# Kernel optimization log

Hardware: AMD Instinct MI355X
Metric: run time of the kernel (lower is better)

The kernel has to match this reference:

```python
import jax, jax.numpy as jnp
import numpy as np

N = 500_000   # rows in embedding matrix
D = 128       # embedding dim
B = 65_536    # number of segments (batches)
SEG = 16      # uniform segment length
T = B * SEG   # total gathered rows


def setup_inputs() -> dict:
    key = jax.random.key(0)
    k1, k2 = jax.random.split(key)
    embs = jax.random.normal(k1, (N, D), dtype=jnp.float32)
    batches = jax.random.randint(k2, (T,), 0, N, dtype=jnp.int32)
    # CSR pointer: [0, 16, 32, ..., T]; monotone, last entry == T, no empty segments
    lens = jnp.arange(B + 1, dtype=jnp.int32) * SEG
    return {"embs": embs, "batches": batches, "lens": lens}


def reference(embs, batches, lens):
    """MultiPool: gather rows then CSR-segmented sum/mean/min/max, concat on dim 1."""
    num_seg = lens.shape[0] - 1
    t = batches.shape[0]
    src = embs[batches]                                   # [T, D] gather
    # CSR pointer -> per-row segment id: seg[i] = j s.t. lens[j] <= i < lens[j+1]
    seg = jnp.searchsorted(lens, jnp.arange(t, dtype=lens.dtype), side="right") - 1
    ssum = jax.ops.segment_sum(src, seg, num_segments=num_seg)                      # [B, D]
    counts = jax.ops.segment_sum(jnp.ones((t,), src.dtype), seg, num_segments=num_seg)
    smean = ssum / jnp.maximum(counts, 1.0)[:, None]
    smin = jax.ops.segment_min(src, seg, num_segments=num_seg)
    smax = jax.ops.segment_max(src, seg, num_segments=num_seg)
    return jnp.concatenate([ssum, smean, smin, smax], axis=1)  # [B, 4*D]
```

## Files before the change

### kernel.cpp

```cpp
#include <hip/hip_runtime.h>
#include <math.h>


#ifndef INFINITY
#define INFINITY __builtin_huge_valf()
#endif

typedef float f32x4 __attribute__((ext_vector_type(4)));

constexpr int D = 128;
constexpr int LANES_PER_SEG = 32;
constexpr int SEGLEN = 16;

__global__ __launch_bounds__(256) void multipool_kernel(
    const float* __restrict__ embs,
    const int*   __restrict__ batches,
    const int*   __restrict__ lens,
    float*       __restrict__ out,
    int B)
{
    const int tid   = blockIdx.x * blockDim.x + threadIdx.x;
    const int seg   = tid >> 5;
    const int lane  = tid & 31;
    if (seg >= B) return;

    const int start = lens[seg];
    const int end   = lens[seg + 1];
    const int cnt   = end - start;

    const int col = lane * 4;

    f32x4 s  = {0.f, 0.f, 0.f, 0.f};
    f32x4 mn = { INFINITY,  INFINITY,  INFINITY,  INFINITY};
    f32x4 mx = {-INFINITY, -INFINITY, -INFINITY, -INFINITY};

    if (cnt == SEGLEN) {
        const int4* ip = reinterpret_cast<const int4*>(batches + start);
        const int4 i0 = ip[0], i1 = ip[1], i2 = ip[2], i3 = ip[3];
        const int rows[SEGLEN] = {i0.x, i0.y, i0.z, i0.w,
                                  i1.x, i1.y, i1.z, i1.w,
                                  i2.x, i2.y, i2.z, i2.w,
                                  i3.x, i3.y, i3.z, i3.w};

        f32x4 v[SEGLEN];
#pragma unroll
        for (int i = 0; i < SEGLEN; ++i) {
            const unsigned off = ((unsigned)rows[i] << 7) | (unsigned)col;
            v[i] = *reinterpret_cast<const f32x4*>(embs + off);
        }
#pragma unroll
        for (int i = 0; i < SEGLEN; ++i) {
            s += v[i];
            mn.x = fminf(mn.x, v[i].x); mn.y = fminf(mn.y, v[i].y);
            mn.z = fminf(mn.z, v[i].z); mn.w = fminf(mn.w, v[i].w);
            mx.x = fmaxf(mx.x, v[i].x); mx.y = fmaxf(mx.y, v[i].y);
            mx.z = fmaxf(mx.z, v[i].z); mx.w = fmaxf(mx.w, v[i].w);
        }
    } else {
        for (int i = start; i < end; ++i) {
            const int row = batches[i];
            const f32x4 v = *reinterpret_cast<const f32x4*>(
                embs + (size_t)row * D + col);
            s += v;
            mn.x = fminf(mn.x, v.x); mn.y = fminf(mn.y, v.y);
            mn.z = fminf(mn.z, v.z); mn.w = fminf(mn.w, v.w);
            mx.x = fmaxf(mx.x, v.x); mx.y = fmaxf(mx.y, v.y);
            mx.z = fmaxf(mx.z, v.z); mx.w = fmaxf(mx.w, v.w);
        }
    }

    const float inv = 1.0f / fmaxf((float)cnt, 1.0f);
    const f32x4 mean = s * inv;

    float* ob = out + (size_t)seg * (4 * D);
    __builtin_nontemporal_store(s,    reinterpret_cast<f32x4*>(ob + col));
    __builtin_nontemporal_store(mean, reinterpret_cast<f32x4*>(ob + D + col));
    __builtin_nontemporal_store(mn,   reinterpret_cast<f32x4*>(ob + 2 * D + col));
    __builtin_nontemporal_store(mx,   reinterpret_cast<f32x4*>(ob + 3 * D + col));
}

extern "C" void kernel_launch(void* const* d_in, const int* in_sizes, int n_in,
                              void* d_out, int out_size, void* d_ws, size_t ws_size,
                              hipStream_t stream) {
    const float* embs    = (const float*)d_in[0];
    const int*   batches = (const int*)d_in[1];
    const int*   lens    = (const int*)d_in[2];
    float*       out     = (float*)d_out;

    const int B = in_sizes[2] - 1;

    const int threads = 256;
    const long long total_threads = (long long)B * LANES_PER_SEG;
    const int blocks = (int)((total_threads + threads - 1) / threads);

    multipool_kernel<<<blocks, threads, 0, stream>>>(embs, batches, lens, out, B);
}
```

Baseline: 101.6 us.

## Map one full wavefront per segment with float2 loads and scalar row indices

Each segment is now handled by a 64-lane wavefront, with two floats per lane, instead of 32 lanes with four floats each. Segment bounds and gathered row indices are moved into scalar registers with readfirstlane, so address math becomes wave-uniform and each row load is one coalesced 512-byte access. This doubles the thread count and halves per-thread work and register use, which should raise occupancy and memory-level parallelism. The cost is more wavefronts to schedule and narrower 8-byte vector accesses per lane.

Result: faster. 95.43 us, median of 2 (-6.1%).

```diff
diff --git a/kernel.cpp b/kernel.cpp
--- a/kernel.cpp
+++ b/kernel.cpp
@@ -6,10 +6,9 @@
 #define INFINITY __builtin_huge_valf()
 #endif
 
-typedef float f32x4 __attribute__((ext_vector_type(4)));
+typedef float f32x2 __attribute__((ext_vector_type(2)));
 
 constexpr int D = 128;
-constexpr int LANES_PER_SEG = 32;
 constexpr int SEGLEN = 16;
 
 __global__ __launch_bounds__(256) void multipool_kernel(
@@ -19,20 +18,20 @@
     float*       __restrict__ out,
     int B)
 {
-    const int tid   = blockIdx.x * blockDim.x + threadIdx.x;
-    const int seg   = tid >> 5;
-    const int lane  = tid & 31;
+    const int tid  = blockIdx.x * blockDim.x + threadIdx.x;
+    const int seg  = tid >> 6;
+    const int lane = threadIdx.x & 63;
     if (seg >= B) return;
 
-    const int start = lens[seg];
-    const int end   = lens[seg + 1];
+    const int start = __builtin_amdgcn_readfirstlane(lens[seg]);
+    const int end   = __builtin_amdgcn_readfirstlane(lens[seg + 1]);
     const int cnt   = end - start;
 
-    const int col = lane * 4;
+    const int col2 = lane * 2;
 
-    f32x4 s  = {0.f, 0.f, 0.f, 0.f};
-    f32x4 mn = { INFINITY,  INFINITY,  INFINITY,  INFINITY};
-    f32x4 mx = {-INFINITY, -INFINITY, -INFINITY, -INFINITY};
+    f32x2 s  = {0.f, 0.f};
+    f32x2 mn = { INFINITY,  INFINITY};
+    f32x2 mx = {-INFINITY, -INFINITY};
 
     if (cnt == SEGLEN) {
         const int4* ip = reinterpret_cast<const int4*>(batches + start);
@@ -42,41 +41,38 @@
                                   i2.x, i2.y, i2.z, i2.w,
                                   i3.x, i3.y, i3.z, i3.w};
 
-        f32x4 v[SEGLEN];
+        f32x2 v[SEGLEN];
 #pragma unroll
         for (int i = 0; i < SEGLEN; ++i) {
-            const unsigned off = ((unsigned)rows[i] << 7) | (unsigned)col;
-            v[i] = *reinterpret_cast<const f32x4*>(embs + off);
+            const int srow = __builtin_amdgcn_readfirstlane(rows[i]);
+            const float* rowp = embs + ((size_t)(unsigned)srow << 7);
+            v[i] = *reinterpret_cast<const f32x2*>(rowp + col2);
         }
 #pragma unroll
         for (int i = 0; i < SEGLEN; ++i) {
             s += v[i];
             mn.x = fminf(mn.x, v[i].x); mn.y = fminf(mn.y, v[i].y);
-            mn.z = fminf(mn.z, v[i].z); mn.w = fminf(mn.w, v[i].w);
             mx.x = fmaxf(mx.x, v[i].x); mx.y = fmaxf(mx.y, v[i].y);
-            mx.z = fmaxf(mx.z, v[i].z); mx.w = fmaxf(mx.w, v[i].w);
         }
     } else {
         for (int i = start; i < end; ++i) {
             const int row = batches[i];
-            const f32x4 v = *reinterpret_cast<const f32x4*>(
-                embs + (size_t)row * D + col);
+            const f32x2 v = *reinterpret_cast<const f32x2*>(
+                embs + (size_t)(unsigned)row * D + col2);
             s += v;
             mn.x = fminf(mn.x, v.x); mn.y = fminf(mn.y, v.y);
-            mn.z = fminf(mn.z, v.z); mn.w = fminf(mn.w, v.w);
             mx.x = fmaxf(mx.x, v.x); mx.y = fmaxf(mx.y, v.y);
-            mx.z = fmaxf(mx.z, v.z); mx.w = fmaxf(mx.w, v.w);
         }
     }
 
     const float inv = 1.0f / fmaxf((float)cnt, 1.0f);
-    const f32x4 mean = s * inv;
+    const f32x2 mean = s * inv;
 
     float* ob = out + (size_t)seg * (4 * D);
-    __builtin_nontemporal_store(s,    reinterpret_cast<f32x4*>(ob + col));
-    __builtin_nontemporal_store(mean, reinterpret_cast<f32x4*>(ob + D + col));
-    __builtin_nontemporal_store(mn,   reinterpret_cast<f32x4*>(ob + 2 * D + col));
-    __builtin_nontemporal_store(mx,   reinterpret_cast<f32x4*>(ob + 3 * D + col));
+    __builtin_nontemporal_store(s,    reinterpret_cast<f32x2*>(ob + col2));
+    __builtin_nontemporal_store(mean, reinterpret_cast<f32x2*>(ob + D + col2));
+    __builtin_nontemporal_store(mn,   reinterpret_cast<f32x2*>(ob + 2 * D + col2));
+    __builtin_nontemporal_store(mx,   reinterpret_cast<f32x2*>(ob + 3 * D + col2));
 }
 
 extern "C" void kernel_launch(void* const* d_in, const int* in_sizes, int n_in,
@@ -90,7 +86,7 @@
     const int B = in_sizes[2] - 1;
 
     const int threads = 256;
-    const long long total_threads = (long long)B * LANES_PER_SEG;
+    const long long total_threads = (long long)B * 64;
     const int blocks = (int)((total_threads + threads - 1) / threads);
 
     multipool_kernel<<<blocks, threads, 0, stream>>>(embs, batches, lens, out, B);
```
